# Performance work log

Hardware: AMD Instinct MI355X
Metric: run time of the kernel (lower is better)

## Reference

```python
import jax, jax.numpy as jnp
import numpy as np

B, T, H = 32, 4096, 128   # batch, seq len, feature dim (ctor L=128)
N = 128                    # S5 state size (S5(dim, dim))
DEPTH = 2                  # L_LT
D_OUT = 64                 # adaptive pool output length (ctor D)
LN_EPS = 1e-5


def setup_inputs() -> dict:
    key = jax.random.key(0)
    ks = iter(jax.random.split(key, 40))
    def nrm(shape, s):
        return (jax.random.normal(next(ks), shape, jnp.float32) * s).astype(jnp.float32)
    inp = {}
    inp['x'] = jax.random.normal(next(ks), (B, T, H), jnp.float32)
    # LayerNorm params (stacked over depth)
    inp['ln1_g'] = jnp.ones((DEPTH, H), jnp.float32)
    inp['ln1_b'] = jnp.zeros((DEPTH, H), jnp.float32)
    inp['ln2_g'] = jnp.ones((DEPTH, H), jnp.float32)
    inp['ln2_b'] = jnp.zeros((DEPTH, H), jnp.float32)
    # S5 params: diagonal complex Lambda, complex B/C, real D skip, per-state log step
    inp['Lam_re'] = -0.5 * jnp.ones((DEPTH, N), jnp.float32)
    inp['Lam_im'] = jnp.tile(jnp.pi * jnp.arange(N, dtype=jnp.float32), (DEPTH, 1))
    inp['B_re'] = nrm((DEPTH, N, H), 1.0 / np.sqrt(H))
    inp['B_im'] = nrm((DEPTH, N, H), 1.0 / np.sqrt(H))
    inp['C_re'] = nrm((DEPTH, H, N), 1.0 / np.sqrt(N))
    inp['C_im'] = nrm((DEPTH, H, N), 1.0 / np.sqrt(N))
    inp['D_skip'] = nrm((DEPTH, H), 1.0)
    inp['log_step'] = jax.random.uniform(next(ks), (DEPTH, N), jnp.float32,
                                         minval=np.log(1e-3), maxval=np.log(1e-1))
    # MLP params
    inp['W1'] = nrm((DEPTH, H, 2 * H), 1.0 / np.sqrt(H))
    inp['b1'] = jnp.zeros((DEPTH, 2 * H), jnp.float32)
    inp['W2'] = nrm((DEPTH, 2 * H, H), 1.0 / np.sqrt(2 * H))
    inp['b2'] = jnp.zeros((DEPTH, H), jnp.float32)
    # Conv1d params (out_ch, in_ch, k=5)
    cs = 1.0 / np.sqrt(H * 5)
    inp['conv1_w'] = nrm((H, H, 5), cs)
    inp['conv1_b'] = jnp.zeros((H,), jnp.float32)
    inp['conv2_w'] = nrm((H, H, 5), cs)
    inp['conv2_b'] = jnp.zeros((H,), jnp.float32)
    return inp


def _layer_norm(x, g, b):
    mu = jnp.mean(x, axis=-1, keepdims=True)
    var = jnp.mean(jnp.square(x - mu), axis=-1, keepdims=True)
    return (x - mu) * jax.lax.rsqrt(var + LN_EPS) * g + b


def _s5(u, lam_re, lam_im, b_re, b_im, c_re, c_im, d_skip, log_step):
    # u: [B, T, H] real. Diagonal S5 with ZOH discretization + parallel scan.
    lam = lam_re + 1j * lam_im                       # (N,) complex
    dt = jnp.exp(log_step)                           # (N,)
    lam_bar = jnp.exp(lam * dt)                      # (N,)
    Bc = b_re + 1j * b_im                            # (N, H)
    B_bar = ((lam_bar - 1.0) / lam)[:, None] * Bc    # (N, H)
    Bu = jnp.einsum('bth,nh->btn', u.astype(jnp.complex64), B_bar)  # [B,T,N]
    A = jnp.broadcast_to(lam_bar.astype(jnp.complex64), Bu.shape)
    def binop(e1, e2):
        a1, x1 = e1
        a2, x2 = e2
        return a1 * a2, a2 * x1 + x2
    _, xs = jax.lax.associative_scan(binop, (A, Bu), axis=1)        # [B,T,N]
    Cc = c_re + 1j * c_im                            # (H, N)
    y = 2.0 * jnp.real(jnp.einsum('btn,hn->bth', xs, Cc)) + u * d_skip
    return y


def _conv1d_s2(x, w, b):
    # x: [B, C, L]; stride 2, padding 2, kernel 5
    y = jax.lax.conv_general_dilated(x, w, window_strides=(2,), padding=[(2, 2)],
                                     dimension_numbers=('NCH', 'OIH', 'NCH'))
    return y + b[None, :, None]


def reference(x, ln1_g, ln1_b, ln2_g, ln2_b, Lam_re, Lam_im, B_re, B_im,
              C_re, C_im, D_skip, log_step, W1, b1, W2, b2,
              conv1_w, conv1_b, conv2_w, conv2_b):
    for i in range(DEPTH):
        # S5 sub-block
        res = x
        xn = _layer_norm(x, ln1_g[i], ln1_b[i])
        x = res + _s5(xn, Lam_re[i], Lam_im[i], B_re[i], B_im[i],
                      C_re[i], C_im[i], D_skip[i], log_step[i])
        # MLP sub-block (dropout = identity in eval)
        res = x
        xn = _layer_norm(x, ln2_g[i], ln2_b[i])
        h = jax.nn.gelu(jnp.einsum('bth,hf->btf', xn, W1[i]) + b1[i], approximate=False)
        x = res + jnp.einsum('btf,fh->bth', h, W2[i]) + b2[i]
    x = jnp.transpose(x, (0, 2, 1))                  # [B, H, T]
    x = jax.nn.relu(_conv1d_s2(x, conv1_w, conv1_b))  # [B, H, T/2]
    x = jax.nn.relu(_conv1d_s2(x, conv2_w, conv2_b))  # [B, H, T/4]
    Lin = x.shape[-1]
    # AdaptiveAvgPool1d(D_OUT): Lin divisible by D_OUT -> uniform windows
    x = x.reshape(x.shape[0], x.shape[1], D_OUT, Lin // D_OUT).mean(axis=-1)
    return x  # [B, H, D_OUT]
```

## Files before the change

### kernel.cpp

```cpp
#include <hip/hip_runtime.h>
#include <math.h>

#define BATCH 32
#define TSEQ  4096
#define HD    128
#define NST   128
#define BT    (BATCH*TSEQ)
#define LC    64
#define NCHK  (TSEQ/LC)

typedef unsigned short bf16;
typedef __attribute__((ext_vector_type(8))) short bf16x8;
typedef __attribute__((ext_vector_type(4))) float f32x4;

__device__ inline float bf2f(bf16 s) {
    union { unsigned int u; float f; } v; v.u = ((unsigned int)s) << 16; return v.f;
}
__device__ inline bf16 f2bf(float f) {
    union { float f; unsigned int u; } v; v.f = f;
    unsigned int u = v.u;
    unsigned int r = (u + 0x7fffu + ((u >> 16) & 1u)) >> 16;
    return (bf16)r;
}
__device__ inline unsigned int pkpair(float lo, float hi) {
    union { float f; unsigned int u; } a, b;
    a.f = lo; b.f = hi;
    return __builtin_amdgcn_perm(b.u + 0x8000u, a.u + 0x8000u, 0x07060302u);
}
__device__ inline bf16x8 pack8f(float4 f0, float4 f1) {
    union { bf16x8 v; unsigned int u[4]; } t;
    t.u[0] = pkpair(f0.x, f0.y);
    t.u[1] = pkpair(f0.z, f0.w);
    t.u[2] = pkpair(f1.x, f1.y);
    t.u[3] = pkpair(f1.z, f1.w);
    return t.v;
}
__device__ inline float2 cmul2(float2 a, float2 b) {
    return make_float2(a.x*b.x - a.y*b.y, a.x*b.y + a.y*b.x);
}
__device__ inline float gelu_f(float x) {
    float u = x*(0.7978845608f + 0.0356774081f*x*x);
    return __fdividef(x, 1.f + __expf(-2.f*u));
}
__device__ inline float2 upk(unsigned int w) {
    union { unsigned int u; float f; } a, b;
    a.u = w << 16; b.u = w & 0xffff0000u;
    return make_float2(a.f, b.f);
}
__device__ inline unsigned int pk(float2 x) { return pkpair(x.x, x.y); }

__global__ void prep_s5(const float* __restrict__ Lam_re, const float* __restrict__ Lam_im,
                        const float* __restrict__ B_re,  const float* __restrict__ B_im,
                        const float* __restrict__ C_re,  const float* __restrict__ C_im,
                        const float* __restrict__ log_step,
                        const float* __restrict__ ln1_g, const float* __restrict__ ln1_b,
                        const float* __restrict__ D_skip,
                        bf16* __restrict__ Wbu_bf,
                        bf16* __restrict__ Wc_bf,
                        float* __restrict__ Sb, float* __restrict__ biasb,
                        float* __restrict__ gd, float* __restrict__ bd,
                        float4* __restrict__ coefs,
                        float2* __restrict__ apow)
{
    int i = blockIdx.x, n = threadIdx.x;
    int in = i*NST + n;
    float lr = Lam_re[in], li = Lam_im[in];
    float dt = expf(log_step[in]);
    float ea = expf(lr*dt);
    float ar = ea*cosf(li*dt), ai = ea*sinf(li*dt);
    float xx = ar - 1.f, yy = ai;
    float den = lr*lr + li*li;
    float sr = (xx*lr + yy*li)/den;
    float si = (yy*lr - xx*li)/den;
    float2 a2 = make_float2(ar, ai);
    float2 p = a2;
    float2* apr = apow + (size_t)i*64*128;
    for (int j = 0; j < 64; ++j) {
        apr[j*128 + n] = p;
        p = cmul2(p, a2);
    }
    float2 q = a2;
    #pragma unroll
    for (int t = 0; t < 6; ++t) q = cmul2(q, q);
    coefs[in] = make_float4(ar, ai, q.x, q.y);

    const float* g  = ln1_g + i*HD;
    const float* bb = ln1_b + i*HD;
    const float* br = B_re + (size_t)in*HD;
    const float* bi = B_im + (size_t)in*HD;
    bf16* wb = Wbu_bf + (size_t)i*256*128;
    float s_re = 0.f, s_im = 0.f, bc_re = 0.f, bc_im = 0.f;
    for (int h = 0; h < HD; ++h) {
        float wre = sr*br[h] - si*bi[h];
        float wim = sr*bi[h] + si*br[h];
        bf16 wrb = f2bf(g[h]*wre), wib = f2bf(g[h]*wim);
        wb[(2*n)*128 + h]   = wrb;
        wb[(2*n+1)*128 + h] = wib;
        s_re += bf2f(wrb); s_im += bf2f(wib);
        bc_re += bb[h]*wre; bc_im += bb[h]*wim;
    }
    Sb[i*256 + 2*n] = s_re;     Sb[i*256 + 2*n+1] = s_im;
    biasb[i*256 + 2*n] = bc_re; biasb[i*256 + 2*n+1] = bc_im;

    const float* cr = C_re + (size_t)i*HD*NST;
    const float* ci = C_im + (size_t)i*HD*NST;
    bf16* wc = Wc_bf + (size_t)i*128*256;
    for (int h = 0; h < HD; ++h) {
        wc[h*256 + 2*n]   = f2bf( 2.f * cr[h*NST + n]);
        wc[h*256 + 2*n+1] = f2bf(-2.f * ci[h*NST + n]);
    }
    gd[i*HD + n] = g[n]*D_skip[i*HD + n];
    bd[i*HD + n] = bb[n]*D_skip[i*HD + n];
}

__global__ void prep_w1(const float* __restrict__ W1, const float* __restrict__ b1,
                        const float* __restrict__ ln2_g, const float* __restrict__ ln2_b,
                        bf16* __restrict__ W1_bf, float* __restrict__ S1,
                        float* __restrict__ bias1p)
{
    int i = blockIdx.x, f = threadIdx.x;
    const float* g  = ln2_g + i*HD;
    const float* bb = ln2_b + i*HD;
    bf16* w = W1_bf + (size_t)i*256*128;
    int j = ((f >> 5) << 5) | (((f >> 2) & 1) << 4) | (((f >> 3) & 3) << 2) | (f & 3);
    float S = 0.f, bi_ = b1[i*256 + f];
    for (int h = 0; h < HD; ++h) {
        float wv = W1[(size_t)i*32768 + h*256 + f];
        bf16 wbv = f2bf(g[h]*wv);
        w[j*128 + h] = wbv;
        S += bf2f(wbv);
        bi_ += bb[h]*wv;
    }
    S1[i*256 + f] = S;
    bias1p[i*256 + f] = bi_;
}

__global__ void prep_w2(const float* __restrict__ W2, bf16* __restrict__ W2_bf)
{
    int i = blockIdx.x, h = threadIdx.x;
    bf16* w = W2_bf + (size_t)i*128*256;
    for (int f = 0; f < 256; ++f)
        w[h*256 + f] = f2bf(W2[(size_t)i*32768 + f*128 + h]);
}

__global__ void prep_wB(const float* __restrict__ w1, const float* __restrict__ w2,
                        bf16* __restrict__ wB1, bf16* __restrict__ wB2)
{
    int idx = blockIdx.x*256 + threadIdx.x;
    if (idx >= 163840) return;
    const float* w = (idx < 81920) ? w1 : w2;
    bf16* wb       = (idx < 81920) ? wB1 : wB2;
    int r   = idx % 81920;
    int c   = r / 640;
    int tap = (r % 640) / 128;
    int ic  = r % 128;
    wb[r] = f2bf(w[(c*128 + ic)*5 + tap]);
}

template<typename TA>
__global__ __launch_bounds__(512, 2) void lngemm2(
    const TA* __restrict__ A,
    const bf16* __restrict__ Bt,
    const float* __restrict__ Svec, const float* __restrict__ bvec,
    bf16* __restrict__ outB,
    float2* __restrict__ munrs)
{
    __shared__ bf16 Bs[256*136];
    __shared__ float Sl[256], bl[256];

    int tid = threadIdx.x;
    #pragma unroll
    for (int it = 0; it < 8; ++it) {
        int f = it*512 + tid;
        int n = f >> 4, kk = (f & 15)*8;
        *(bf16x8*)&Bs[n*136 + kk] = *(const bf16x8*)(Bt + n*128 + kk);
    }
    if (tid < 256) { Sl[tid] = Svec[tid]; bl[tid] = bvec[tid]; }
    __syncthreads();

    int wid = tid >> 6, lane = tid & 63;
    int quad = lane >> 4, cl = lane & 15;
    int s0 = blockIdx.x*16 + wid*2;
    size_t row0 = (size_t)s0*16 + cl;

    bf16x8 af[2][4];
    float mu[2], rs[2], mr[2];
    #pragma unroll
    for (int p = 0; p < 2; ++p) {
        size_t row = row0 + (size_t)p*16;
        float sm = 0.f, sq = 0.f;
        if constexpr (sizeof(TA) == 2) {
            const bf16* ar = (const bf16*)A + row*128;
            #pragma unroll
            for (int ks = 0; ks < 4; ++ks) {
                af[p][ks] = *(const bf16x8*)(ar + quad*8 + ks*32);
                union { bf16x8 v; unsigned int u[4]; } aa; aa.v = af[p][ks];
                #pragma unroll
                for (int jp = 0; jp < 4; ++jp) {
                    float2 vv = upk(aa.u[jp]);
                    sm += vv.x + vv.y;
                    sq += vv.x*vv.x + vv.y*vv.y;
                }
            }
        } else {
            const float* ar = (const float*)A + row*128;
            #pragma unroll
            for (int ks = 0; ks < 4; ++ks) {
                float4 f0 = *(const float4*)(ar + quad*8 + ks*32);
                float4 f1 = *(const float4*)(ar + quad*8 + ks*32 + 4);
                sm += f0.x + f0.y + f0.z + f0.w + f1.x + f1.y + f1.z + f1.w;
                sq += f0.x*f0.x + f0.y*f0.y + f0.z*f0.z + f0.w*f0.w
                    + f1.x*f1.x + f1.y*f1.y + f1.z*f1.z + f1.w*f1.w;
                af[p][ks] = pack8f(f0, f1);
            }
        }
        sm += __shfl_xor(sm, 16); sm += __shfl_xor(sm, 32);
        sq += __shfl_xor(sq, 16); sq += __shfl_xor(sq, 32);
        mu[p] = sm * (1.f/128.f);
        rs[p] = rsqrtf(sq*(1.f/128.f) - mu[p]*mu[p] + 1e-5f);
        mr[p] = mu[p]*rs[p];
        if (quad == 0) munrs[row] = make_float2(mu[p], rs[p]);
    }

    #pragma unroll
    for (int g = 0; g < 4; ++g) {
        f32x4 acc0[4] = {}, acc1[4] = {};
        #pragma unroll
        for (int t4 = 0; t4 < 4; ++t4) {
            const bf16* wrp = &Bs[(((g*4+t4)*16) + cl)*136 + quad*8];
            #pragma unroll
            for (int ks = 0; ks < 4; ++ks) {
                bf16x8 w = *(const bf16x8*)(wrp + ks*32);
                acc0[t4] = __builtin_amdgcn_mfma_f32_16x16x32_bf16(w, af[0][ks], acc0[t4], 0, 0, 0);
                acc1[t4] = __builtin_amdgcn_mfma_f32_16x16x32_bf16(w, af[1][ks], acc1[t4], 0, 0, 0);
            }
        }
        #pragma unroll
        for (int t4 = 0; t4 < 4; ++t4) {
            int n0 = (g*4+t4)*16 + quad*4;
            float4 S4 = *(const float4*)&Sl[n0];
            float4 b4 = *(const float4*)&bl[n0];
            float4 o;
            o.x = rs[0]*acc0[t4][0] - mr[0]*S4.x + b4.x;
            o.y = rs[0]*acc0[t4][1] - mr[0]*S4.y + b4.y;
            o.z = rs[0]*acc0[t4][2] - mr[0]*S4.z + b4.z;
            o.w = rs[0]*acc0[t4][3] - mr[0]*S4.w + b4.w;
            *(uint2*)(outB + row0*256 + n0) = make_uint2(pkpair(o.x, o.y), pkpair(o.z, o.w));
            o.x = rs[1]*acc1[t4][0] - mr[1]*S4.x + b4.x;
            o.y = rs[1]*acc1[t4][1] - mr[1]*S4.y + b4.y;
            o.z = rs[1]*acc1[t4][2] - mr[1]*S4.z + b4.z;
            o.w = rs[1]*acc1[t4][3] - mr[1]*S4.w + b4.w;
            *(uint2*)(outB + (row0+16)*256 + n0) = make_uint2(pkpair(o.x, o.y), pkpair(o.z, o.w));
        }
    }
}

template<typename TR>
__global__ __launch_bounds__(512, 2) void gemm2s(
    const bf16* __restrict__ A,
    const bf16* __restrict__ Bt,
    bf16* out,
    const TR* resid,
    const float2* __restrict__ munrs,
    const float* __restrict__ gdp, const float* __restrict__ bdp,
    const float2* __restrict__ carry,
    const float2* __restrict__ apow)
{
    __shared__ bf16 Bs[128*264];
    __shared__ float gdl[128], bdl[128];

    int tid = threadIdx.x;
    #pragma unroll
    for (int it = 0; it < 8; ++it) {
        int f = it*512 + tid;
        int n = f >> 5, kk = (f & 31)*8;
        *(bf16x8*)&Bs[n*264 + kk] = *(const bf16x8*)(Bt + n*256 + kk);
    }
    if (tid < 128) { gdl[tid] = gdp[tid]; bdl[tid] = bdp[tid]; }
    __syncthreads();

    int wid = tid >> 6, lane = tid & 63;
    int quad = lane >> 4, cl = lane & 15;
    int s0 = blockIdx.x*16 + wid*2;
    size_t row0 = (size_t)s0*16 + cl;

    bf16x8 af[2][8];
    float mu[2], rs[2];
    #pragma unroll
    for (int p = 0; p < 2; ++p) {
        size_t row = row0 + (size_t)p*16;
        float2 m2 = munrs[row]; mu[p] = m2.x; rs[p] = m2.y;
        const bf16* ar = A + row*256 + quad*8;
        int b  = (int)(row >> 12);
        int tp = (int)(row & 4095);
        int cc = tp >> 6, j = tp & 63;
        const float2* cin = carry + (size_t)cc*(BATCH*NST) + (size_t)b*NST;
        const float2* ap  = apow + (size_t)j*128;
        #pragma unroll
        for (int ks = 0; ks < 8; ++ks) {
            union { bf16x8 v; unsigned int u[4]; } t;
            t.v = *(const bf16x8*)(ar + ks*32);
            int n0 = quad*4 + ks*16;
            #pragma unroll
            for (int jp = 0; jp < 4; ++jp) {
                float2 v  = upk(t.u[jp]);
                float2 ad = cmul2(ap[n0+jp], cin[n0+jp]);
                t.u[jp] = pk(make_float2(v.x + ad.x, v.y + ad.y));
            }
            af[p][ks] = t.v;
        }
    }

    ushort4 rvh[2][8];
    if constexpr (sizeof(TR) == 2) {
        #pragma unroll
        for (int p = 0; p < 2; ++p)
            #pragma unroll
            for (int nt = 0; nt < 8; ++nt)
                rvh[p][nt] = *(const ushort4*)((const bf16*)resid
                               + (row0 + (size_t)p*16)*128 + nt*16 + quad*4);
    }

    #pragma unroll
    for (int nt = 0; nt < 8; ++nt) {
        const bf16* wrp = &Bs[(nt*16 + cl)*264 + quad*8];
        f32x4 a0 = {}, a1 = {};
        #pragma unroll
        for (int ks = 0; ks < 8; ++ks) {
            bf16x8 w = *(const bf16x8*)(wrp + ks*32);
            a0 = __builtin_amdgcn_mfma_f32_16x16x32_bf16(w, af[0][ks], a0, 0, 0, 0);
            a1 = __builtin_amdgcn_mfma_f32_16x16x32_bf16(w, af[1][ks], a1, 0, 0, 0);
        }
        int n0 = nt*16 + quad*4;
        float4 g4 = *(const float4*)&gdl[n0];
        float4 b4 = *(const float4*)&bdl[n0];
        #pragma unroll
        for (int p = 0; p < 2; ++p) {
            f32x4 ac = p ? a1 : a0;
            size_t oidx = (row0 + (size_t)p*16)*128 + n0;
            float4 rv;
            if constexpr (sizeof(TR) == 2) {
                ushort4 u4 = rvh[p][nt];
                rv = make_float4(bf2f(u4.x), bf2f(u4.y), bf2f(u4.z), bf2f(u4.w));
            } else {
                rv = *(const float4*)((const float*)resid + oidx);
            }
            float4 o;
            o.x = rv.x + ac[0] + (rv.x - mu[p])*rs[p]*g4.x + b4.x;
            o.y = rv.y + ac[1] + (rv.y - mu[p])*rs[p]*g4.y + b4.y;
            o.z = rv.z + ac[2] + (rv.z - mu[p])*rs[p]*g4.z + b4.z;
            o.w = rv.w + ac[3] + (rv.w - mu[p])*rs[p]*g4.w + b4.w;
            *(uint2*)(out + oidx) = make_uint2(pkpair(o.x, o.y), pkpair(o.z, o.w));
        }
    }
}

__global__ __launch_bounds__(1024, 2) void mlp_fused(
    const bf16* X,
    const bf16* __restrict__ W1t,
    const bf16* __restrict__ W2t,
    const float* __restrict__ S1v, const float* __restrict__ b1v,
    const float* __restrict__ b2v,
    bf16* out)
{
    __shared__ bf16 As1[256*136];
    __shared__ bf16 Bs2[128*264];
    __shared__ float S1l[256], b1l[256], b2l[128];

    int tid = threadIdx.x;
    #pragma unroll
    for (int it = 0; it < 4; ++it) {
        int f = it*1024 + tid;
        int n = f >> 4, kk = (f & 15)*8;
        *(bf16x8*)&As1[n*136 + kk] = *(const bf16x8*)(W1t + n*128 + kk);
    }
    #pragma unroll
    for (int it = 0; it < 4; ++it) {
        int f = it*1024 + tid;
        int n = f >> 5, kk = (f & 31)*8;
        *(bf16x8*)&Bs2[n*264 + kk] = *(const bf16x8*)(W2t + n*256 + kk);
    }
    if (tid < 256)      { S1l[tid] = S1v[tid]; b1l[tid] = b1v[tid]; }
    else if (tid < 384) { int h = tid - 256; b2l[h] = b2v[h]; }
    __syncthreads();

    int wid = tid >> 6, lane = tid & 63;
    int quad = lane >> 4, cl = lane & 15;
    int s = blockIdx.x*16 + wid;
    size_t row = (size_t)s*16 + cl;

    const bf16* ar = X + row*128;
    bf16x8 af[4];
    float sm = 0.f, sq = 0.f;
    #pragma unroll
    for (int ks = 0; ks < 4; ++ks) {
        af[ks] = *(const bf16x8*)(ar + quad*8 + ks*32);
        union { bf16x8 v; unsigned int u[4]; } aa; aa.v = af[ks];
        #pragma unroll
        for (int jp = 0; jp < 4; ++jp) {
            float2 vv = upk(aa.u[jp]);
            sm += vv.x + vv.y;
            sq += vv.x*vv.x + vv.y*vv.y;
        }
    }
    sm += __shfl_xor(sm, 16); sm += __shfl_xor(sm, 32);
    sq += __shfl_xor(sq, 16); sq += __shfl_xor(sq, 32);
    float mu = sm * (1.f/128.f);
    float rs = rsqrtf(sq*(1.f/128.f) - mu*mu + 1e-5f);
    float mr = mu*rs;

    union { unsigned int u[16][2]; bf16x8 v[8]; } hp;
    #pragma unroll
    for (int half = 0; half < 2; ++half) {
        f32x4 acc[8] = {};
        #pragma unroll
        for (int nt = 0; nt < 8; ++nt) {
            const bf16* wrp = &As1[(((half*8+nt)*16) + cl)*136 + quad*8];
            #pragma unroll
            for (int ks = 0; ks < 4; ++ks)
                acc[nt] = __builtin_amdgcn_mfma_f32_16x16x32_bf16(
                              *(const bf16x8*)(wrp + ks*32), af[ks], acc[nt], 0, 0, 0);
        }
        #pragma unroll
        for (int nt = 0; nt < 8; ++nt) {
            int NT = half*8 + nt;
            int fb = ((NT >> 1) << 5) + (quad << 3) + ((NT & 1) << 2);
            float4 S4 = *(const float4*)&S1l[fb];
            float4 b4 = *(const float4*)&b1l[fb];
            float4 o;
            o.x = gelu_f(rs*acc[nt][0] - mr*S4.x + b4.x);
            o.y = gelu_f(rs*acc[nt][1] - mr*S4.y + b4.y);
            o.z = gelu_f(rs*acc[nt][2] - mr*S4.z + b4.z);
            o.w = gelu_f(rs*acc[nt][3] - mr*S4.w + b4.w);
            hp.u[NT][0] = pkpair(o.x, o.y);
            hp.u[NT][1] = pkpair(o.z, o.w);
        }
    }

    #pragma unroll
    for (int nt = 0; nt < 8; ++nt) {
        const bf16* wrp = &Bs2[(nt*16 + cl)*264 + quad*8];
        f32x4 a0 = {};
        #pragma unroll
        for (int ks = 0; ks < 8; ++ks) {
            bf16x8 w = *(const bf16x8*)(wrp + ks*32);
            a0 = __builtin_amdgcn_mfma_f32_16x16x32_bf16(w, hp.v[ks], a0, 0, 0, 0);
        }
        int n0 = nt*16 + quad*4;
        size_t oidx = row*128 + n0;
        float4 b4 = *(const float4*)&b2l[n0];
        ushort4 u4 = *(const ushort4*)(X + oidx);
        float4 o;
        o.x = a0[0] + b4.x + bf2f(u4.x);
        o.y = a0[1] + b4.y + bf2f(u4.y);
        o.z = a0[2] + b4.z + bf2f(u4.z);
        o.w = a0[3] + b4.w + bf2f(u4.w);
        *(uint2*)(out + oidx) = make_uint2(pkpair(o.x, o.y), pkpair(o.z, o.w));
    }
}

__global__ __launch_bounds__(256) void scan_local(uint2* __restrict__ xs,
                                                  const float4* __restrict__ coefs,
                                                  float2* __restrict__ carry)
{
    int flat = blockIdx.x*256 + threadIdx.x;
    int n2 = flat & 63;
    int b = (flat >> 6) & 31;
    int c = flat >> 11;
    float4 cf0 = coefs[2*n2], cf1 = coefs[2*n2+1];
    float2 a0 = make_float2(cf0.x, cf0.y);
    float2 a1 = make_float2(cf1.x, cf1.y);
    uint2* base = xs + ((size_t)(b*TSEQ + c*LC))*64 + n2;
    float2 x0 = make_float2(0.f, 0.f), x1 = make_float2(0.f, 0.f);
    uint2 v = base[0];
    #pragma unroll 4
    for (int j = 0; j < LC; ++j) {
        uint2 vc = v;
        if (j + 1 < LC) v = base[(size_t)(j+1)*64];
        float2 v0 = upk(vc.x), v1 = upk(vc.y);
        x0 = make_float2(a0.x*x0.x - a0.y*x0.y + v0.x, a0.x*x0.y + a0.y*x0.x + v0.y);
        x1 = make_float2(a1.x*x1.x - a1.y*x1.y + v1.x, a1.x*x1.y + a1.y*x1.x + v1.y);
        base[(size_t)j*64] = make_uint2(pk(x0), pk(x1));
    }
    carry[c*(BATCH*NST) + b*NST + 2*n2]   = x0;
    carry[c*(BATCH*NST) + b*NST + 2*n2+1] = x1;
}

__global__ void scan_carry(float2* __restrict__ carry, const float4* __restrict__ coefs)
{
    int flat = blockIdx.x*256 + threadIdx.x;
    int n = flat & 127;
    float4 cf = coefs[n];
    float2 aL = make_float2(cf.z, cf.w);
    float2 x = make_float2(0.f, 0.f);
    for (int c = 0; c < NCHK; ++c) {
        float2* p = carry + c*(BATCH*NST) + flat;
        float2 v = *p;
        *p = x;
        x = make_float2(aL.x*x.x - aL.y*x.y + v.x, aL.x*x.y + aL.y*x.x + v.y);
    }
}

__global__ __launch_bounds__(256, 4) void conv1_mfma(
    const bf16* __restrict__ X,
    const bf16* __restrict__ wB,
    const float* __restrict__ bias,
    bf16* __restrict__ out,
    int Tin, int Lout)
{
    __shared__ bf16 As[128][72];
    __shared__ bf16 Bs[128][72];
    int tid  = threadIdx.x;
    int lane = tid & 63;
    int wave = tid >> 6;
    int wm = wave >> 1, wn = wave & 1;
    int quad = lane >> 4, cl = lane & 15;
    int row0 = blockIdx.x * 128;
    int b  = row0 / Lout;
    int l0 = row0 % Lout;
    const bf16* Xb = X + (size_t)b*Tin*128;

    f32x4 acc[4][4] = {};

    for (int k0 = 0; k0 < 640; k0 += 64) {
        int tap = k0 / 128;
        int icb = k0 % 128;
        #pragma unroll
        for (int it = 0; it < 4; ++it) {
            int idx = it*256 + tid;
            int r = idx >> 3, kof = (idx & 7) * 8;
            int t = 2*(l0 + r) - 2 + tap;
            bf16x8 z = {0,0,0,0,0,0,0,0};
            if (t >= 0 && t < Tin) z = *(const bf16x8*)(Xb + (size_t)t*128 + icb + kof);
            *(bf16x8*)&As[r][kof] = z;
        }
        #pragma unroll
        for (int it = 0; it < 4; ++it) {
            int idx = it*256 + tid;
            int n = idx >> 3, kof = (idx & 7) * 8;
            *(bf16x8*)&Bs[n][kof] = *(const bf16x8*)(wB + (size_t)n*640 + k0 + kof);
        }
        __syncthreads();
        #pragma unroll
        for (int kk = 0; kk < 64; kk += 32) {
            bf16x8 af[4], bfr[4];
            #pragma unroll
            for (int i = 0; i < 4; ++i)
                af[i] = *(const bf16x8*)&As[wm*64 + i*16 + cl][kk + quad*8];
            #pragma unroll
            for (int j = 0; j < 4; ++j)
                bfr[j] = *(const bf16x8*)&Bs[wn*64 + j*16 + cl][kk + quad*8];
            #pragma unroll
            for (int i = 0; i < 4; ++i)
                #pragma unroll
                for (int j = 0; j < 4; ++j)
                    acc[i][j] = __builtin_amdgcn_mfma_f32_16x16x32_bf16(
                                    bfr[j], af[i], acc[i][j], 0, 0, 0);
        }
        __syncthreads();
    }

    #pragma unroll
    for (int i = 0; i < 4; ++i) {
        int grow = row0 + wm*64 + i*16 + cl;
        #pragma unroll
        for (int j = 0; j < 4; ++j) {
            int gcol = wn*64 + j*16 + quad*4;
            float4 bv = *(const float4*)(bias + gcol);
            float4 t;
            t.x = fmaxf(acc[i][j][0] + bv.x, 0.f); t.y = fmaxf(acc[i][j][1] + bv.y, 0.f);
            t.z = fmaxf(acc[i][j][2] + bv.z, 0.f); t.w = fmaxf(acc[i][j][3] + bv.w, 0.f);
            uint2 pu = make_uint2(pkpair(t.x, t.y), pkpair(t.z, t.w));
            *(uint2*)(out + (size_t)grow*128 + gcol) = pu;
        }
    }
}

__global__ __launch_bounds__(256, 4) void conv2_pool(
    const bf16* __restrict__ X,
    const bf16* __restrict__ wB,
    const float* __restrict__ bias,
    float* __restrict__ outp,
    int Tin, int Lout)
{
    __shared__ bf16 As[128][72];
    __shared__ bf16 Bs[128][72];
    int tid  = threadIdx.x;
    int lane = tid & 63;
    int wave = tid >> 6;
    int wm = wave >> 1, wn = wave & 1;
    int quad = lane >> 4, cl = lane & 15;
    int row0 = blockIdx.x * 128;
    int b  = row0 / Lout;
    int l0 = row0 % Lout;
    int d0 = l0 / 16;
    const bf16* Xb = X + (size_t)b*Tin*128;

    f32x4 acc[4][4] = {};

    for (int k0 = 0; k0 < 640; k0 += 64) {
        int tap = k0 / 128;
        int icb = k0 % 128;
        #pragma unroll
        for (int it = 0; it < 4; ++it) {
            int idx = it*256 + tid;
            int r = idx >> 3, kof = (idx & 7) * 8;
            int t = 2*(l0 + r) - 2 + tap;
            bf16x8 z = {0,0,0,0,0,0,0,0};
            if (t >= 0 && t < Tin) z = *(const bf16x8*)(Xb + (size_t)t*128 + icb + kof);
            *(bf16x8*)&As[r][kof] = z;
        }
        #pragma unroll
        for (int it = 0; it < 4; ++it) {
            int idx = it*256 + tid;
            int n = idx >> 3, kof = (idx & 7) * 8;
            *(bf16x8*)&Bs[n][kof] = *(const bf16x8*)(wB + (size_t)n*640 + k0 + kof);
        }
        __syncthreads();
        #pragma unroll
        for (int kk = 0; kk < 64; kk += 32) {
            bf16x8 af[4], bfr[4];
            #pragma unroll
            for (int i = 0; i < 4; ++i)
                af[i] = *(const bf16x8*)&As[wm*64 + i*16 + cl][kk + quad*8];
            #pragma unroll
            for (int j = 0; j < 4; ++j)
                bfr[j] = *(const bf16x8*)&Bs[wn*64 + j*16 + cl][kk + quad*8];
            #pragma unroll
            for (int i = 0; i < 4; ++i)
                #pragma unroll
                for (int j = 0; j < 4; ++j)
                    acc[i][j] = __builtin_amdgcn_mfma_f32_16x16x32_bf16(
                                    bfr[j], af[i], acc[i][j], 0, 0, 0);
        }
        __syncthreads();
    }

    #pragma unroll
    for (int j = 0; j < 4; ++j) {
        int gcol = wn*64 + j*16 + quad*4;
        float4 bv = *(const float4*)(bias + gcol);
        #pragma unroll
        for (int i = 0; i < 4; ++i) {
            float4 sp;
            sp.x = fmaxf(acc[i][j][0] + bv.x, 0.f);
            sp.y = fmaxf(acc[i][j][1] + bv.y, 0.f);
            sp.z = fmaxf(acc[i][j][2] + bv.z, 0.f);
            sp.w = fmaxf(acc[i][j][3] + bv.w, 0.f);
            #pragma unroll
            for (int off = 1; off <= 8; off <<= 1) {
                sp.x += __shfl_xor(sp.x, off);
                sp.y += __shfl_xor(sp.y, off);
                sp.z += __shfl_xor(sp.z, off);
                sp.w += __shfl_xor(sp.w, off);
            }
            if (cl == 0) {
                int d = d0 + wm*4 + i;
                float* op = outp + (size_t)b*8192 + (size_t)gcol*64 + d;
                op[0]   = sp.x * (1.f/16.f);
                op[64]  = sp.y * (1.f/16.f);
                op[128] = sp.z * (1.f/16.f);
                op[192] = sp.w * (1.f/16.f);
            }
        }
    }
}

extern "C" void kernel_launch(void* const* d_in, const int* in_sizes, int n_in,
                              void* d_out, int out_size, void* d_ws, size_t ws_size,
                              hipStream_t stream)
{
    (void)in_sizes; (void)n_in; (void)out_size; (void)ws_size;
    const float* x_in    = (const float*)d_in[0];
    const float* ln1_g   = (const float*)d_in[1];
    const float* ln1_b   = (const float*)d_in[2];
    const float* ln2_g   = (const float*)d_in[3];
    const float* ln2_b   = (const float*)d_in[4];
    const float* Lam_re  = (const float*)d_in[5];
    const float* Lam_im  = (const float*)d_in[6];
    const float* B_re    = (const float*)d_in[7];
    const float* B_im    = (const float*)d_in[8];
    const float* C_re    = (const float*)d_in[9];
    const float* C_im    = (const float*)d_in[10];
    const float* D_skip  = (const float*)d_in[11];
    const float* log_step= (const float*)d_in[12];
    const float* W1      = (const float*)d_in[13];
    const float* b1      = (const float*)d_in[14];
    const float* W2      = (const float*)d_in[15];
    const float* b2      = (const float*)d_in[16];
    const float* conv1_w = (const float*)d_in[17];
    const float* conv1_b = (const float*)d_in[18];
    const float* conv2_w = (const float*)d_in[19];
    const float* conv2_b = (const float*)d_in[20];
    float* out = (float*)d_out;

    char* ws = (char*)d_ws;
    bf16*   Xbf    = (bf16*) (ws);
    bf16*   Cbuf   = (bf16*) (ws + (size_t)33554432);
    bf16*   Cv1    = (bf16*) (ws + (size_t)100663296);
    float2* munrs  = (float2*)(ws + (size_t)117440512);
    char*   wreg   = ws + (size_t)118489088;
    bf16*   Wbu_bf = (bf16*)(wreg);
    bf16*   Wc_bf  = (bf16*)(wreg + 131072);
    bf16*   W1_bf  = (bf16*)(wreg + 262144);
    bf16*   W2_bf  = (bf16*)(wreg + 393216);
    float*  Sb     = (float*)(wreg + 524288);
    float*  biasb  = (float*)(wreg + 526336);
    float*  S1     = (float*)(wreg + 528384);
    float*  bias1p = (float*)(wreg + 530432);
    float*  gd     = (float*)(wreg + 532480);
    float*  bd     = (float*)(wreg + 533504);
    float4* coefs  = (float4*)(wreg + 534528);
    bf16*   wB1    = (bf16*)(wreg + 538624);
    bf16*   wB2    = (bf16*)(wreg + 702464);
    float2* carry  = (float2*)(wreg + 866304);
    float2* apow   = (float2*)(wreg + 2963456);

    prep_s5<<<2, 128, 0, stream>>>(Lam_re, Lam_im, B_re, B_im, C_re, C_im, log_step,
                                   ln1_g, ln1_b, D_skip,
                                   Wbu_bf, Wc_bf, Sb, biasb, gd, bd, coefs, apow);
    prep_w1<<<2, 256, 0, stream>>>(W1, b1, ln2_g, ln2_b, W1_bf, S1, bias1p);
    prep_w2<<<2, 128, 0, stream>>>(W2, W2_bf);
    prep_wB<<<640, 256, 0, stream>>>(conv1_w, conv2_w, wB1, wB2);

    for (int i = 0; i < 2; ++i) {
        if (i == 0)
            lngemm2<float><<<512, 512, 0, stream>>>(
                x_in, Wbu_bf, Sb, biasb, Cbuf, munrs);
        else
            lngemm2<bf16><<<512, 512, 0, stream>>>(
                Xbf, Wbu_bf + 32768, Sb + 256, biasb + 256, Cbuf, munrs);
        scan_local<<<512, 256, 0, stream>>>((uint2*)Cbuf, coefs + i*NST, carry);
        scan_carry<<<16, 256, 0, stream>>>(carry, coefs + i*NST);
        if (i == 0)
            gemm2s<float><<<512, 512, 0, stream>>>(
                Cbuf, Wc_bf, Xbf, x_in, munrs, gd, bd, carry, apow);
        else
            gemm2s<bf16><<<512, 512, 0, stream>>>(
                Cbuf, Wc_bf + 32768, Xbf, Xbf, munrs, gd + 128, bd + 128,
                carry, apow + 64*128);
        mlp_fused<<<512, 1024, 0, stream>>>(
            Xbf, W1_bf + (size_t)i*32768, W2_bf + (size_t)i*32768,
            S1 + i*256, bias1p + i*256, b2 + i*HD, Xbf);
    }

    conv1_mfma<<<512, 256, 0, stream>>>(Xbf, wB1, conv1_b, Cv1, 4096, 2048);
    conv2_pool<<<256, 256, 0, stream>>>(Cv1, wB2, conv2_b, out, 2048, 1024);
}
```

Before: 522.1 us.

## Stage GEMM weights through LDS in halves to raise occupancy

The three GEMM kernels (LN+GEMM, S5 output GEMM, fused MLP) now load their weight matrices into shared memory in two halves instead of all at once. This halves their LDS footprint, and launch bounds are raised to allow four 512-thread blocks per CU, with the aim of getting more resident waves to hide memory latency. In exchange, each block reloads weight tiles from global memory and adds extra __syncthreads barriers between phases. More blocks per CU also tightens the per-thread register budget, which risks spills given the large register-held A fragments.

```diff
diff --git a/kernel.cpp b/kernel.cpp
--- a/kernel.cpp
+++ b/kernel.cpp
@@ -158,25 +158,18 @@
 }
 
 template<typename TA>
-__global__ __launch_bounds__(512, 2) void lngemm2(
+__global__ __launch_bounds__(512, 4) void lngemm2(
     const TA* __restrict__ A,
     const bf16* __restrict__ Bt,
     const float* __restrict__ Svec, const float* __restrict__ bvec,
     bf16* __restrict__ outB,
     float2* __restrict__ munrs)
 {
-    __shared__ bf16 Bs[256*136];
+    __shared__ bf16 Bs[128*136];
     __shared__ float Sl[256], bl[256];
 
     int tid = threadIdx.x;
-    #pragma unroll
-    for (int it = 0; it < 8; ++it) {
-        int f = it*512 + tid;
-        int n = f >> 4, kk = (f & 15)*8;
-        *(bf16x8*)&Bs[n*136 + kk] = *(const bf16x8*)(Bt + n*128 + kk);
-    }
     if (tid < 256) { Sl[tid] = Svec[tid]; bl[tid] = bvec[tid]; }
-    __syncthreads();
 
     int wid = tid >> 6, lane = tid & 63;
     int quad = lane >> 4, cl = lane & 15;
@@ -223,40 +216,53 @@
     }
 
     #pragma unroll
-    for (int g = 0; g < 4; ++g) {
-        f32x4 acc0[4] = {}, acc1[4] = {};
-        #pragma unroll
-        for (int t4 = 0; t4 < 4; ++t4) {
-            const bf16* wrp = &Bs[(((g*4+t4)*16) + cl)*136 + quad*8];
-            #pragma unroll
-            for (int ks = 0; ks < 4; ++ks) {
-                bf16x8 w = *(const bf16x8*)(wrp + ks*32);
-                acc0[t4] = __builtin_amdgcn_mfma_f32_16x16x32_bf16(w, af[0][ks], acc0[t4], 0, 0, 0);
-                acc1[t4] = __builtin_amdgcn_mfma_f32_16x16x32_bf16(w, af[1][ks], acc1[t4], 0, 0, 0);
-            }
-        }
-        #pragma unroll
-        for (int t4 = 0; t4 < 4; ++t4) {
-            int n0 = (g*4+t4)*16 + quad*4;
-            float4 S4 = *(const float4*)&Sl[n0];
-            float4 b4 = *(const float4*)&bl[n0];
-            float4 o;
-            o.x = rs[0]*acc0[t4][0] - mr[0]*S4.x + b4.x;
-            o.y = rs[0]*acc0[t4][1] - mr[0]*S4.y + b4.y;
-            o.z = rs[0]*acc0[t4][2] - mr[0]*S4.z + b4.z;
-            o.w = rs[0]*acc0[t4][3] - mr[0]*S4.w + b4.w;
-            *(uint2*)(outB + row0*256 + n0) = make_uint2(pkpair(o.x, o.y), pkpair(o.z, o.w));
-            o.x = rs[1]*acc1[t4][0] - mr[1]*S4.x + b4.x;
-            o.y = rs[1]*acc1[t4][1] - mr[1]*S4.y + b4.y;
-            o.z = rs[1]*acc1[t4][2] - mr[1]*S4.z + b4.z;
-            o.w = rs[1]*acc1[t4][3] - mr[1]*S4.w + b4.w;
-            *(uint2*)(outB + (row0+16)*256 + n0) = make_uint2(pkpair(o.x, o.y), pkpair(o.z, o.w));
+    for (int h = 0; h < 2; ++h) {
+        if (h) __syncthreads();
+        #pragma unroll
+        for (int it = 0; it < 4; ++it) {
+            int f = it*512 + tid;
+            int n = f >> 4, kk = (f & 15)*8;
+            *(bf16x8*)&Bs[n*136 + kk] = *(const bf16x8*)(Bt + (h*128 + n)*128 + kk);
+        }
+        __syncthreads();
+
+        #pragma unroll
+        for (int gl = 0; gl < 2; ++gl) {
+            int g = h*2 + gl;
+            f32x4 acc0[4] = {}, acc1[4] = {};
+            #pragma unroll
+            for (int t4 = 0; t4 < 4; ++t4) {
+                const bf16* wrp = &Bs[(((gl*4+t4)*16) + cl)*136 + quad*8];
+                #pragma unroll
+                for (int ks = 0; ks < 4; ++ks) {
+                    bf16x8 w = *(const bf16x8*)(wrp + ks*32);
+                    acc0[t4] = __builtin_amdgcn_mfma_f32_16x16x32_bf16(w, af[0][ks], acc0[t4], 0, 0, 0);
+                    acc1[t4] = __builtin_amdgcn_mfma_f32_16x16x32_bf16(w, af[1][ks], acc1[t4], 0, 0, 0);
+                }
+            }
+            #pragma unroll
+            for (int t4 = 0; t4 < 4; ++t4) {
+                int n0 = (g*4+t4)*16 + quad*4;
+                float4 S4 = *(const float4*)&Sl[n0];
+                float4 b4 = *(const float4*)&bl[n0];
+                float4 o;
+                o.x = rs[0]*acc0[t4][0] - mr[0]*S4.x + b4.x;
+                o.y = rs[0]*acc0[t4][1] - mr[0]*S4.y + b4.y;
+                o.z = rs[0]*acc0[t4][2] - mr[0]*S4.z + b4.z;
+                o.w = rs[0]*acc0[t4][3] - mr[0]*S4.w + b4.w;
+                *(uint2*)(outB + row0*256 + n0) = make_uint2(pkpair(o.x, o.y), pkpair(o.z, o.w));
+                o.x = rs[1]*acc1[t4][0] - mr[1]*S4.x + b4.x;
+                o.y = rs[1]*acc1[t4][1] - mr[1]*S4.y + b4.y;
+                o.z = rs[1]*acc1[t4][2] - mr[1]*S4.z + b4.z;
+                o.w = rs[1]*acc1[t4][3] - mr[1]*S4.w + b4.w;
+                *(uint2*)(outB + (row0+16)*256 + n0) = make_uint2(pkpair(o.x, o.y), pkpair(o.z, o.w));
+            }
         }
     }
 }
 
 template<typename TR>
-__global__ __launch_bounds__(512, 2) void gemm2s(
+__global__ __launch_bounds__(512, 4) void gemm2s(
     const bf16* __restrict__ A,
     const bf16* __restrict__ Bt,
     bf16* out,
@@ -266,18 +272,11 @@
     const float2* __restrict__ carry,
     const float2* __restrict__ apow)
 {
-    __shared__ bf16 Bs[128*264];
+    __shared__ bf16 Bs[64*264];
     __shared__ float gdl[128], bdl[128];
 
     int tid = threadIdx.x;
-    #pragma unroll
-    for (int it = 0; it < 8; ++it) {
-        int f = it*512 + tid;
-        int n = f >> 5, kk = (f & 31)*8;
-        *(bf16x8*)&Bs[n*264 + kk] = *(const bf16x8*)(Bt + n*256 + kk);
-    }
     if (tid < 128) { gdl[tid] = gdp[tid]; bdl[tid] = bdp[tid]; }
-    __syncthreads();
 
     int wid = tid >> 6, lane = tid & 63;
     int quad = lane >> 4, cl = lane & 15;
@@ -322,35 +321,48 @@
     }
 
     #pragma unroll
-    for (int nt = 0; nt < 8; ++nt) {
-        const bf16* wrp = &Bs[(nt*16 + cl)*264 + quad*8];
-        f32x4 a0 = {}, a1 = {};
-        #pragma unroll
-        for (int ks = 0; ks < 8; ++ks) {
-            bf16x8 w = *(const bf16x8*)(wrp + ks*32);
-            a0 = __builtin_amdgcn_mfma_f32_16x16x32_bf16(w, af[0][ks], a0, 0, 0, 0);
-            a1 = __builtin_amdgcn_mfma_f32_16x16x32_bf16(w, af[1][ks], a1, 0, 0, 0);
-        }
-        int n0 = nt*16 + quad*4;
-        float4 g4 = *(const float4*)&gdl[n0];
-        float4 b4 = *(const float4*)&bdl[n0];
-        #pragma unroll
-        for (int p = 0; p < 2; ++p) {
-            f32x4 ac = p ? a1 : a0;
-            size_t oidx = (row0 + (size_t)p*16)*128 + n0;
-            float4 rv;
-            if constexpr (sizeof(TR) == 2) {
-                ushort4 u4 = rvh[p][nt];
-                rv = make_float4(bf2f(u4.x), bf2f(u4.y), bf2f(u4.z), bf2f(u4.w));
-            } else {
-                rv = *(const float4*)((const float*)resid + oidx);
-            }
-            float4 o;
-            o.x = rv.x + ac[0] + (rv.x - mu[p])*rs[p]*g4.x + b4.x;
-            o.y = rv.y + ac[1] + (rv.y - mu[p])*rs[p]*g4.y + b4.y;
-            o.z = rv.z + ac[2] + (rv.z - mu[p])*rs[p]*g4.z + b4.z;
-            o.w = rv.w + ac[3] + (rv.w - mu[p])*rs[p]*g4.w + b4.w;
-            *(uint2*)(out + oidx) = make_uint2(pkpair(o.x, o.y), pkpair(o.z, o.w));
+    for (int h = 0; h < 2; ++h) {
+        if (h) __syncthreads();
+        #pragma unroll
+        for (int it = 0; it < 4; ++it) {
+            int f = it*512 + tid;
+            int n = f >> 5, kk = (f & 31)*8;
+            *(bf16x8*)&Bs[n*264 + kk] = *(const bf16x8*)(Bt + (size_t)(h*64 + n)*256 + kk);
+        }
+        __syncthreads();
+
+        #pragma unroll
+        for (int ntl = 0; ntl < 4; ++ntl) {
+            int nt = h*4 + ntl;
+            const bf16* wrp = &Bs[(ntl*16 + cl)*264 + quad*8];
+            f32x4 a0 = {}, a1 = {};
+            #pragma unroll
+            for (int ks = 0; ks < 8; ++ks) {
+                bf16x8 w = *(const bf16x8*)(wrp + ks*32);
+                a0 = __builtin_amdgcn_mfma_f32_16x16x32_bf16(w, af[0][ks], a0, 0, 0, 0);
+                a1 = __builtin_amdgcn_mfma_f32_16x16x32_bf16(w, af[1][ks], a1, 0, 0, 0);
+            }
+            int n0 = nt*16 + quad*4;
+            float4 g4 = *(const float4*)&gdl[n0];
+            float4 b4 = *(const float4*)&bdl[n0];
+            #pragma unroll
+            for (int p = 0; p < 2; ++p) {
+                f32x4 ac = p ? a1 : a0;
+                size_t oidx = (row0 + (size_t)p*16)*128 + n0;
+                float4 rv;
+                if constexpr (sizeof(TR) == 2) {
+                    ushort4 u4 = rvh[p][nt];
+                    rv = make_float4(bf2f(u4.x), bf2f(u4.y), bf2f(u4.z), bf2f(u4.w));
+                } else {
+                    rv = *(const float4*)((const float*)resid + oidx);
+                }
+                float4 o;
+                o.x = rv.x + ac[0] + (rv.x - mu[p])*rs[p]*g4.x + b4.x;
+                o.y = rv.y + ac[1] + (rv.y - mu[p])*rs[p]*g4.y + b4.y;
+                o.z = rv.z + ac[2] + (rv.z - mu[p])*rs[p]*g4.z + b4.z;
+                o.w = rv.w + ac[3] + (rv.w - mu[p])*rs[p]*g4.w + b4.w;
+                *(uint2*)(out + oidx) = make_uint2(pkpair(o.x, o.y), pkpair(o.z, o.w));
+            }
         }
     }
 }
@@ -363,26 +375,13 @@
     const float* __restrict__ b2v,
     bf16* out)
 {
-    __shared__ bf16 As1[256*136];
-    __shared__ bf16 Bs2[128*264];
+    __shared__ bf16 As1[128*136];
+    __shared__ bf16 Bs2[64*264];
     __shared__ float S1l[256], b1l[256], b2l[128];
 
     int tid = threadIdx.x;
-    #pragma unroll
-    for (int it = 0; it < 4; ++it) {
-        int f = it*1024 + tid;
-        int n = f >> 4, kk = (f & 15)*8;
-        *(bf16x8*)&As1[n*136 + kk] = *(const bf16x8*)(W1t + n*128 + kk);
-    }
-    #pragma unroll
-    for (int it = 0; it < 4; ++it) {
-        int f = it*1024 + tid;
-        int n = f >> 5, kk = (f & 31)*8;
-        *(bf16x8*)&Bs2[n*264 + kk] = *(const bf16x8*)(W2t + n*256 + kk);
-    }
     if (tid < 256)      { S1l[tid] = S1v[tid]; b1l[tid] = b1v[tid]; }
     else if (tid < 384) { int h = tid - 256; b2l[h] = b2v[h]; }
-    __syncthreads();
 
     int wid = tid >> 6, lane = tid & 63;
     int quad = lane >> 4, cl = lane & 15;
@@ -412,10 +411,18 @@
     union { unsigned int u[16][2]; bf16x8 v[8]; } hp;
     #pragma unroll
     for (int half = 0; half < 2; ++half) {
+        if (half) __syncthreads();
+        #pragma unroll
+        for (int it = 0; it < 2; ++it) {
+            int f = it*1024 + tid;
+            int n = f >> 4, kk = (f & 15)*8;
+            *(bf16x8*)&As1[n*136 + kk] = *(const bf16x8*)(W1t + (half*128 + n)*128 + kk);
+        }
+        __syncthreads();
         f32x4 acc[8] = {};
         #pragma unroll
         for (int nt = 0; nt < 8; ++nt) {
-            const bf16* wrp = &As1[(((half*8+nt)*16) + cl)*136 + quad*8];
+            const bf16* wrp = &As1[((nt*16) + cl)*136 + quad*8];
             #pragma unroll
             for (int ks = 0; ks < 4; ++ks)
                 acc[nt] = __builtin_amdgcn_mfma_f32_16x16x32_bf16(
@@ -438,24 +445,36 @@
     }
 
     #pragma unroll
-    for (int nt = 0; nt < 8; ++nt) {
-        const bf16* wrp = &Bs2[(nt*16 + cl)*264 + quad*8];
-        f32x4 a0 = {};
-        #pragma unroll
-        for (int ks = 0; ks < 8; ++ks) {
-            bf16x8 w = *(const bf16x8*)(wrp + ks*32);
-            a0 = __builtin_amdgcn_mfma_f32_16x16x32_bf16(w, hp.v[ks], a0, 0, 0, 0);
-        }
-        int n0 = nt*16 + quad*4;
-        size_t oidx = row*128 + n0;
-        float4 b4 = *(const float4*)&b2l[n0];
-        ushort4 u4 = *(const ushort4*)(X + oidx);
-        float4 o;
-        o.x = a0[0] + b4.x + bf2f(u4.x);
-        o.y = a0[1] + b4.y + bf2f(u4.y);
-        o.z = a0[2] + b4.z + bf2f(u4.z);
-        o.w = a0[3] + b4.w + bf2f(u4.w);
-        *(uint2*)(out + oidx) = make_uint2(pkpair(o.x, o.y), pkpair(o.z, o.w));
+    for (int h2 = 0; h2 < 2; ++h2) {
+        __syncthreads();
+        #pragma unroll
+        for (int it = 0; it < 2; ++it) {
+            int f = it*1024 + tid;
+            int n = f >> 5, kk = (f & 31)*8;
+            *(bf16x8*)&Bs2[n*264 + kk] = *(const bf16x8*)(W2t + (size_t)(h2*64 + n)*256 + kk);
+        }
+        __syncthreads();
+        #pragma unroll
+        for (int ntl = 0; ntl < 4; ++ntl) {
+            int nt = h2*4 + ntl;
+            const bf16* wrp = &Bs2[(ntl*16 + cl)*264 + quad*8];
+            f32x4 a0 = {};
+            #pragma unroll
+            for (int ks = 0; ks < 8; ++ks) {
+                bf16x8 w = *(const bf16x8*)(wrp + ks*32);
+                a0 = __builtin_amdgcn_mfma_f32_16x16x32_bf16(w, hp.v[ks], a0, 0, 0, 0);
+            }
+            int n0 = nt*16 + quad*4;
+            size_t oidx = row*128 + n0;
+            float4 b4 = *(const float4*)&b2l[n0];
+            ushort4 u4 = *(const ushort4*)(X + oidx);
+            float4 o;
+            o.x = a0[0] + b4.x + bf2f(u4.x);
+            o.y = a0[1] + b4.y + bf2f(u4.y);
+            o.z = a0[2] + b4.z + bf2f(u4.z);
+            o.w = a0[3] + b4.w + bf2f(u4.w);
+            *(uint2*)(out + oidx) = make_uint2(pkpair(o.x, o.y), pkpair(o.z, o.w));
+        }
     }
 }
 
```

After: 589.3 us. 1.13x slower.
